# Performance work log

Hardware: AMD Instinct MI355X
Metric: run time of the kernel (lower is better)

## Reference

```python
import jax, jax.numpy as jnp
import numpy as np
from jax import lax

SEQ, BATCH, IN, HID = 4096, 8, 1024, 1024


def setup_inputs() -> dict:
    key = jax.random.key(0)
    k1, k2 = jax.random.split(key)
    X = jax.random.normal(k1, (SEQ, BATCH, IN), dtype=jnp.float32)
    hidden = jnp.zeros((BATCH, HID), dtype=jnp.float32)  # None init == zeros
    W = jax.random.normal(k2, (3 * HID, IN), dtype=jnp.float32) * 0.02
    b = jnp.zeros((3 * HID,), dtype=jnp.float32)
    return {"X": X, "hidden": hidden, "W": W, "b": b}


def reference(X, hidden, W, b):
    # window=1: source = X; Y = Linear(X) -> [S, B, 3H]
    Y = jnp.einsum('sbi,hi->sbh', X, W) + b
    Z, F, O = jnp.split(Y, 3, axis=2)
    Z = jnp.tanh(Z)
    F = jax.nn.sigmoid(F)

    # ForgetMult: c_t = f_t * z_t + (1 - f_t) * c_{t-1}
    def step(c, fz):
        f, z = fz
        c = f * z + (1.0 - f) * c
        return c, c

    _, C = lax.scan(step, hidden, (F, Z))  # C: [S, B, H]
    H = jax.nn.sigmoid(O) * C
    return (H, C[-1:, :, :], C)
```

## Files before the change

### kernel.cpp

```cpp
#include <hip/hip_runtime.h>
#include <hip/hip_bf16.h>
#include <stdint.h>

#define S_   4096
#define B_   8
#define IN_  1024
#define H_   1024
#define M_   (S_ * B_)
#define N_   (3 * H_)
#define K_   IN_
#define CH_  (B_ * H_)
#define NC_  256
#define T_   (S_ / NC_)
#define STRD (CH_ / 4)

typedef unsigned short u16;
typedef __bf16 bf16x8 __attribute__((ext_vector_type(8)));
typedef float  f32x4  __attribute__((ext_vector_type(4)));

__device__ __forceinline__ u16 f2bf(float f) {
  unsigned u = __float_as_uint(f);
  u += 0x7fffu + ((u >> 16) & 1u);
  return (u16)(u >> 16);
}

__device__ __forceinline__ float sigmoid_(float x) { return 1.0f / (1.0f + __expf(-x)); }
__device__ __forceinline__ float tanh_(float x)    { return 2.0f / (1.0f + __expf(-2.0f * x)) - 1.0f; }

__global__ void cvt_all(const float* __restrict__ X, const float* __restrict__ W,
                        u16* __restrict__ Xb, u16* __restrict__ Wb) {
  const int nX = M_ * K_ / 8, nW = N_ * K_ / 8;
  int i = blockIdx.x * blockDim.x + threadIdx.x;
  const float* in; u16* out; int j;
  if (i < nX)           { in = X; out = Xb; j = i; }
  else if (i < nX + nW) { in = W; out = Wb; j = i - nX; }
  else return;
  const float4* p = (const float4*)in;
  float4 a = p[2 * j], b = p[2 * j + 1];
  alignas(16) u16 us[8] = {f2bf(a.x), f2bf(a.y), f2bf(a.z), f2bf(a.w),
                           f2bf(b.x), f2bf(b.y), f2bf(b.z), f2bf(b.w)};
  ((uint4*)out)[j] = *(const uint4*)us;
}

#define SWZ(x) ((x) ^ (((x) >> 3) & 0x30))

#define DS_A(s, h, mh) do {                                                    \
  const char* base_ = (const char*)As_[(s)*2+(h)];                             \
  af[0] = *(const bf16x8*)(base_ + aoff[mh][0]);                               \
  af[1] = *(const bf16x8*)(base_ + aoff[mh][1]);                               \
  af[2] = *(const bf16x8*)(base_ + aoff[mh][2]);                               \
  af[3] = *(const bf16x8*)(base_ + aoff[mh][3]);                               \
} while (0)

#define DS_B(s, h) do {                                                        \
  const char* base_ = (const char*)Bs_[(s)*2+(h)];                             \
  bfr[0] = *(const bf16x8*)(base_ + boff[0]);                                  \
  bfr[1] = *(const bf16x8*)(base_ + boff[1]);                                  \
  bfr[2] = *(const bf16x8*)(base_ + boff[2]);                                  \
  bfr[3] = *(const bf16x8*)(base_ + boff[3]);                                  \
} while (0)

#define MMA(mh) do {                                                           \
  __builtin_amdgcn_s_setprio(1);                                              \
  _Pragma("unroll")                                                            \
  for (int fi_ = 0; fi_ < 4; ++fi_)                                            \
    _Pragma("unroll")                                                          \
    for (int fj_ = 0; fj_ < 4; ++fj_)                                          \
      acc[(mh)*4+fi_][fj_] = __builtin_amdgcn_mfma_f32_16x16x32_bf16(          \
          af[fi_], bfr[fj_], acc[(mh)*4+fi_][fj_], 0, 0, 0);                   \
  __builtin_amdgcn_s_setprio(0);                                              \
} while (0)

#define PH_SYNC() do {                                                         \
  asm volatile("" ::: "memory");                                               \
  __builtin_amdgcn_s_barrier();                                                \
  asm volatile("s_waitcnt lgkmcnt(0)" ::: "memory");                           \
} while (0)

#define PH_END() do {                                                          \
  asm volatile("" ::: "memory");                                               \
  __builtin_amdgcn_s_barrier();                                                \
} while (0)

#define VW(n) asm volatile("s_waitcnt vmcnt(" #n ")" ::: "memory")

__global__ __launch_bounds__(512, 2) void gemm_act(
    const u16* __restrict__ Ab, const u16* __restrict__ Bb,
    const float* __restrict__ bias,
    float* __restrict__ zt,
    float* __restrict__ Cf,
    float* __restrict__ Ho) {
  __shared__ alignas(16) u16 As_[4][8192];
  __shared__ alignas(16) u16 Bs_[4][8192];

  const int tid = threadIdx.x;
  const int w = tid >> 6, l = tid & 63;
  const int m0 = blockIdx.y * 256, n0 = blockIdx.x * 256;
  const int wmo = (w >> 2) * 128, wno = (w & 3) * 64;
  const int lr = l & 15, lq = l >> 4;

  const int D0b  = w * 1024 + l * 16;
  const int row0 = D0b >> 6;
  const int c0   = (SWZ(D0b) & 63) >> 1;

  int aoff[2][4], boff[4];
#pragma unroll
  for (int mh = 0; mh < 2; ++mh)
#pragma unroll
    for (int fi = 0; fi < 4; ++fi)
      aoff[mh][fi] = SWZ((wmo + (mh * 4 + fi) * 16 + lr) * 64 + lq * 16);
#pragma unroll
  for (int fj = 0; fj < 4; ++fj)
    boff[fj] = SWZ((wno + fj * 16 + lr) * 64 + lq * 16);

  auto stage = [&](const u16* __restrict__ G, int rb, int tt, int hh, u16* dstp) {
    const u16* s0 = G + (size_t)(rb + row0) * K_ + (tt * 64 + hh * 32 + c0);
    __builtin_amdgcn_global_load_lds(
        (const __attribute__((address_space(1))) void*)s0,
        (__attribute__((address_space(3))) void*)(dstp + (D0b >> 1)), 16, 0, 0);
    const u16* s1 = s0 + (size_t)128 * K_;
    __builtin_amdgcn_global_load_lds(
        (const __attribute__((address_space(1))) void*)s1,
        (__attribute__((address_space(3))) void*)(dstp + (D0b >> 1) + 4096), 16, 0, 0);
  };

  f32x4 acc[8][4] = {};
  bf16x8 af[4], bfr[4];

  stage(Ab, m0, 0, 0, As_[0]); stage(Bb, n0, 0, 0, Bs_[0]);
  stage(Ab, m0, 0, 1, As_[1]); stage(Bb, n0, 0, 1, Bs_[1]);
  stage(Ab, m0, 1, 0, As_[2]); stage(Bb, n0, 1, 0, Bs_[2]);
  VW(4);
  PH_END();

  for (int i = 0; i < 7; ++i) {
    const int t1 = 2 * i + 1, t2 = 2 * i + 2, t3 = 2 * i + 3;
    DS_A(0, 0, 0); DS_B(0, 0); stage(Ab, m0, t1, 1, As_[3]);
    PH_SYNC(); MMA(0); PH_END();
    DS_A(0, 0, 1);             stage(Bb, n0, t1, 1, Bs_[3]);
    PH_SYNC(); MMA(1); PH_END();
    DS_A(0, 1, 0); DS_B(0, 1); stage(Ab, m0, t2, 0, As_[0]);
    PH_SYNC(); MMA(0); PH_END();
    DS_A(0, 1, 1);             stage(Bb, n0, t2, 0, Bs_[0]); VW(4);
    PH_SYNC(); MMA(1); PH_END();
    DS_A(1, 0, 0); DS_B(1, 0); stage(Ab, m0, t2, 1, As_[1]);
    PH_SYNC(); MMA(0); PH_END();
    DS_A(1, 0, 1);             stage(Bb, n0, t2, 1, Bs_[1]);
    PH_SYNC(); MMA(1); PH_END();
    DS_A(1, 1, 0); DS_B(1, 1); stage(Ab, m0, t3, 0, As_[2]);
    PH_SYNC(); MMA(0); PH_END();
    DS_A(1, 1, 1);             stage(Bb, n0, t3, 0, Bs_[2]); VW(4);
    PH_SYNC(); MMA(1); PH_END();
  }

  DS_A(0, 0, 0); DS_B(0, 0); stage(Ab, m0, 15, 1, As_[3]);
  PH_SYNC(); MMA(0); PH_END();
  DS_A(0, 0, 1);             stage(Bb, n0, 15, 1, Bs_[3]);
  PH_SYNC(); MMA(1); PH_END();
  DS_A(0, 1, 0); DS_B(0, 1);
  PH_SYNC(); MMA(0); PH_END();
  DS_A(0, 1, 1); VW(0);
  PH_SYNC(); MMA(1); PH_END();
  DS_A(1, 0, 0); DS_B(1, 0);
  PH_SYNC(); MMA(0); PH_END();
  DS_A(1, 0, 1);
  PH_SYNC(); MMA(1); PH_END();
  DS_A(1, 1, 0); DS_B(1, 1);
  PH_SYNC(); MMA(0); PH_END();
  DS_A(1, 1, 1);
  PH_SYNC(); MMA(1); PH_END();

  const int seg = n0 >> 10;
  const int nh0 = (n0 & 1023) + wno;
  float* dst = (seg == 0) ? zt : (seg == 1 ? Cf : Ho);
#pragma unroll
  for (int fj = 0; fj < 4; ++fj) {
    const int nn = nh0 + fj * 16 + lr;
    const float bv = bias[seg * 1024 + nn];
#pragma unroll
    for (int fi = 0; fi < 8; ++fi) {
#pragma unroll
      for (int rr = 0; rr < 4; ++rr) {
        const int mm = m0 + wmo + fi * 16 + lq * 4 + rr;
        const float v = acc[fi][fj][rr] + bv;
        dst[(size_t)mm * H_ + nn] = (seg == 0) ? tanh_(v) : sigmoid_(v);
      }
    }
  }
}


#define UPDA4(ff, zz) do { float om_;                                          \
  om_ = 1.f - (ff).x; c.x = (ff).x * (zz).x + om_ * c.x; A.x *= om_;           \
  om_ = 1.f - (ff).y; c.y = (ff).y * (zz).y + om_ * c.y; A.y *= om_;           \
  om_ = 1.f - (ff).z; c.z = (ff).z * (zz).z + om_ * c.z; A.z *= om_;           \
  om_ = 1.f - (ff).w; c.w = (ff).w * (zz).w + om_ * c.w; A.w *= om_;           \
} while (0)

#define UPDB4(ff, zz) do {                                                     \
  c.x = (ff).x * (zz).x + (1.f - (ff).x) * c.x;                                \
  c.y = (ff).y * (zz).y + (1.f - (ff).y) * c.y;                                \
  c.z = (ff).z * (zz).z + (1.f - (ff).z) * c.z;                                \
  c.w = (ff).w * (zz).w + (1.f - (ff).w) * c.w;                                \
} while (0)

__global__ void scanA(const float* __restrict__ Cf, const float* __restrict__ zt,
                      float* __restrict__ ckA, float* __restrict__ ckC) {
  const int ch4 = blockIdx.x * 256 + threadIdx.x;
  const int j   = blockIdx.y;
  const float4* __restrict__ Cf4 = (const float4*)Cf;
  const float4* __restrict__ zt4 = (const float4*)zt;
  size_t base = (size_t)j * T_ * STRD + ch4;
  float4 A = {1.f, 1.f, 1.f, 1.f}, c = {0.f, 0.f, 0.f, 0.f};
  float4 f0 = Cf4[base],        z0 = zt4[base];
  float4 f1 = Cf4[base + STRD], z1 = zt4[base + STRD];
#pragma unroll
  for (int tt = 0; tt < T_ - 2; ++tt) {
    const float4 fn = Cf4[base + 2 * STRD];
    const float4 zn = zt4[base + 2 * STRD];
    UPDA4(f0, z0);
    f0 = f1; z0 = z1; f1 = fn; z1 = zn;
    base += STRD;
  }
  UPDA4(f0, z0);
  UPDA4(f1, z1);
  ((float4*)ckA)[(size_t)j * STRD + ch4] = A;
  ((float4*)ckC)[(size_t)j * STRD + ch4] = c;
}

__global__ void scanComb(const float* __restrict__ ckA, const float* __restrict__ ckC,
                         const float* __restrict__ hidden, float* __restrict__ carry) {
  const int ch4 = blockIdx.x * 64 + threadIdx.x;
  const float4* __restrict__ a4 = (const float4*)ckA;
  const float4* __restrict__ c4 = (const float4*)ckC;
  float4* __restrict__ cr4 = (float4*)carry;
  float4 c = ((const float4*)hidden)[ch4];
  float4 A0 = a4[ch4], C0 = c4[ch4];
#pragma unroll 8
  for (int j = 0; j < NC_ - 1; ++j) {
    const float4 A1 = a4[(size_t)(j + 1) * STRD + ch4];
    const float4 C1 = c4[(size_t)(j + 1) * STRD + ch4];
    cr4[(size_t)j * STRD + ch4] = c;
    c.x = C0.x + A0.x * c.x;
    c.y = C0.y + A0.y * c.y;
    c.z = C0.z + A0.z * c.z;
    c.w = C0.w + A0.w * c.w;
    A0 = A1; C0 = C1;
  }
  cr4[(size_t)(NC_ - 1) * STRD + ch4] = c;
}

__global__ void scanB(float* __restrict__ Cf,
                      const float* __restrict__ zt,
                      float* __restrict__ Ho,
                      float* __restrict__ Clast,
                      const float* __restrict__ carry) {
  const int ch4 = blockIdx.x * 256 + threadIdx.x;
  const int j   = blockIdx.y;
  float4* __restrict__ Cf4 = (float4*)Cf;
  const float4* __restrict__ zt4 = (const float4*)zt;
  float4* __restrict__ Ho4 = (float4*)Ho;
  size_t base = (size_t)j * T_ * STRD + ch4;
  float4 c = ((const float4*)carry)[(size_t)j * STRD + ch4];
  float4 f0 = Cf4[base],        z0 = zt4[base],        o0 = Ho4[base];
  float4 f1 = Cf4[base + STRD], z1 = zt4[base + STRD], o1 = Ho4[base + STRD];
#pragma unroll
  for (int tt = 0; tt < T_ - 2; ++tt) {
    const float4 fn = Cf4[base + 2 * STRD];
    const float4 zn = zt4[base + 2 * STRD];
    const float4 on = Ho4[base + 2 * STRD];
    UPDB4(f0, z0);
    Cf4[base] = c;
    Ho4[base] = float4{o0.x * c.x, o0.y * c.y, o0.z * c.z, o0.w * c.w};
    f0 = f1; z0 = z1; o0 = o1; f1 = fn; z1 = zn; o1 = on;
    base += STRD;
  }
  UPDB4(f0, z0);
  Cf4[base] = c;
  Ho4[base] = float4{o0.x * c.x, o0.y * c.y, o0.z * c.z, o0.w * c.w};
  base += STRD;
  UPDB4(f1, z1);
  Cf4[base] = c;
  Ho4[base] = float4{o1.x * c.x, o1.y * c.y, o1.z * c.z, o1.w * c.w};
  if (j == NC_ - 1) ((float4*)Clast)[ch4] = c;
}

extern "C" void kernel_launch(void* const* d_in, const int* in_sizes, int n_in,
                              void* d_out, int out_size, void* d_ws, size_t ws_size,
                              hipStream_t stream) {
  const float* X    = (const float*)d_in[0];
  const float* hid  = (const float*)d_in[1];
  const float* W    = (const float*)d_in[2];
  const float* bias = (const float*)d_in[3];

  float* out   = (float*)d_out;
  float* Ho    = out;
  float* Clast = out + (size_t)M_ * H_;
  float* Cf    = Clast + CH_;

  char* ws = (char*)d_ws;
  u16*  Xb    = (u16*)ws;
  u16*  Wb    = (u16*)(ws + 67108864);
  float* zt   = (float*)(ws + 73400320);
  float* ckA  = (float*)(ws);
  float* ckC  = (float*)(ws + 8388608);
  float* carry= (float*)(ws + 16777216);

  const int nAll = M_ * K_ / 8 + N_ * K_ / 8;
  cvt_all<<<(nAll + 255) / 256, 256, 0, stream>>>(X, W, Xb, Wb);
  gemm_act<<<dim3(N_ / 256, M_ / 256), 512, 0, stream>>>(Xb, Wb, bias, zt, Cf, Ho);
  scanA<<<dim3(CH_ / 1024, NC_), 256, 0, stream>>>(Cf, zt, ckA, ckC);
  scanComb<<<CH_ / 4 / 64, 64, 0, stream>>>(ckA, ckC, hid, carry);
  scanB<<<dim3(CH_ / 1024, NC_), 256, 0, stream>>>(Cf, zt, Ho, Clast, carry);
}
```

Measured before the change: 835.3 us.

## Store gate activations as fp16 and widen scan chunks with 8-wide lanes

The GEMM epilogue now writes the tanh(Z) and sigmoid(F) intermediates as fp16 into separate workspace buffers instead of fp32, cutting the bytes written by the GEMM and read twice by the scan kernels. The scan kernels process 8 channels per thread with fp16 vector loads, and the chunk count drops from 256 to 64, so each thread does longer serial runs with fewer blocks. This lowers memory traffic in the bandwidth-bound scan phases. It costs precision in the recurrence inputs and reduces parallelism per scan launch, with the inner loop no longer fully unrolled.

```diff
diff --git a/kernel.cpp b/kernel.cpp
--- a/kernel.cpp
+++ b/kernel.cpp
@@ -10,13 +10,15 @@
 #define N_   (3 * H_)
 #define K_   IN_
 #define CH_  (B_ * H_)
-#define NC_  256
+#define NC_  64
 #define T_   (S_ / NC_)
-#define STRD (CH_ / 4)
+#define STR8 (CH_ / 8)
+#define STR4 (CH_ / 4)
 
 typedef unsigned short u16;
 typedef __bf16 bf16x8 __attribute__((ext_vector_type(8)));
 typedef float  f32x4  __attribute__((ext_vector_type(4)));
+typedef _Float16 h8   __attribute__((ext_vector_type(8)));
 
 __device__ __forceinline__ u16 f2bf(float f) {
   unsigned u = __float_as_uint(f);
@@ -87,8 +89,8 @@
 __global__ __launch_bounds__(512, 2) void gemm_act(
     const u16* __restrict__ Ab, const u16* __restrict__ Bb,
     const float* __restrict__ bias,
-    float* __restrict__ zt,
-    float* __restrict__ Cf,
+    _Float16* __restrict__ zh,
+    _Float16* __restrict__ fh,
     float* __restrict__ Ho) {
   __shared__ alignas(16) u16 As_[4][8192];
   __shared__ alignas(16) u16 Bs_[4][8192];
@@ -172,7 +174,6 @@
 
   const int seg = n0 >> 10;
   const int nh0 = (n0 & 1023) + wno;
-  float* dst = (seg == 0) ? zt : (seg == 1 ? Cf : Ho);
 #pragma unroll
   for (int fj = 0; fj < 4; ++fj) {
     const int nn = nh0 + fj * 16 + lr;
@@ -183,49 +184,54 @@
       for (int rr = 0; rr < 4; ++rr) {
         const int mm = m0 + wmo + fi * 16 + lq * 4 + rr;
         const float v = acc[fi][fj][rr] + bv;
-        dst[(size_t)mm * H_ + nn] = (seg == 0) ? tanh_(v) : sigmoid_(v);
+        const size_t idx = (size_t)mm * H_ + nn;
+        if (seg == 0)      zh[idx] = (_Float16)tanh_(v);
+        else if (seg == 1) fh[idx] = (_Float16)sigmoid_(v);
+        else               Ho[idx] = sigmoid_(v);
       }
     }
   }
 }
 
 
-#define UPDA4(ff, zz) do { float om_;                                          \
-  om_ = 1.f - (ff).x; c.x = (ff).x * (zz).x + om_ * c.x; A.x *= om_;           \
-  om_ = 1.f - (ff).y; c.y = (ff).y * (zz).y + om_ * c.y; A.y *= om_;           \
-  om_ = 1.f - (ff).z; c.z = (ff).z * (zz).z + om_ * c.z; A.z *= om_;           \
-  om_ = 1.f - (ff).w; c.w = (ff).w * (zz).w + om_ * c.w; A.w *= om_;           \
-} while (0)
-
-#define UPDB4(ff, zz) do {                                                     \
-  c.x = (ff).x * (zz).x + (1.f - (ff).x) * c.x;                                \
-  c.y = (ff).y * (zz).y + (1.f - (ff).y) * c.y;                                \
-  c.z = (ff).z * (zz).z + (1.f - (ff).z) * c.z;                                \
-  c.w = (ff).w * (zz).w + (1.f - (ff).w) * c.w;                                \
-} while (0)
-
-__global__ void scanA(const float* __restrict__ Cf, const float* __restrict__ zt,
+__global__ void scanA(const _Float16* __restrict__ fhp, const _Float16* __restrict__ zhp,
                       float* __restrict__ ckA, float* __restrict__ ckC) {
-  const int ch4 = blockIdx.x * 256 + threadIdx.x;
+  const int ch8 = blockIdx.x * 256 + threadIdx.x;
   const int j   = blockIdx.y;
-  const float4* __restrict__ Cf4 = (const float4*)Cf;
-  const float4* __restrict__ zt4 = (const float4*)zt;
-  size_t base = (size_t)j * T_ * STRD + ch4;
-  float4 A = {1.f, 1.f, 1.f, 1.f}, c = {0.f, 0.f, 0.f, 0.f};
-  float4 f0 = Cf4[base],        z0 = zt4[base];
-  float4 f1 = Cf4[base + STRD], z1 = zt4[base + STRD];
-#pragma unroll
+  const h8* __restrict__ fh = (const h8*)fhp;
+  const h8* __restrict__ zh = (const h8*)zhp;
+  size_t base = (size_t)j * T_ * STR8 + ch8;
+  float A[8], c[8];
+#pragma unroll
+  for (int k = 0; k < 8; ++k) { A[k] = 1.f; c[k] = 0.f; }
+  h8 f0 = fh[base],        z0 = zh[base];
+  h8 f1 = fh[base + STR8], z1 = zh[base + STR8];
   for (int tt = 0; tt < T_ - 2; ++tt) {
-    const float4 fn = Cf4[base + 2 * STRD];
-    const float4 zn = zt4[base + 2 * STRD];
-    UPDA4(f0, z0);
-    f0 = f1; z0 = z1; f1 = fn; z1 = zn;
-    base += STRD;
-  }
-  UPDA4(f0, z0);
-  UPDA4(f1, z1);
-  ((float4*)ckA)[(size_t)j * STRD + ch4] = A;
-  ((float4*)ckC)[(size_t)j * STRD + ch4] = c;
+    const h8 f2 = fh[base + 2 * STR8];
+    const h8 z2 = zh[base + 2 * STR8];
+#pragma unroll
+    for (int k = 0; k < 8; ++k) {
+      const float f = (float)f0[k], z = (float)z0[k], om = 1.f - f;
+      c[k] = f * z + om * c[k]; A[k] *= om;
+    }
+    f0 = f1; z0 = z1; f1 = f2; z1 = z2; base += STR8;
+  }
+#pragma unroll
+  for (int k = 0; k < 8; ++k) {
+    const float f = (float)f0[k], z = (float)z0[k], om = 1.f - f;
+    c[k] = f * z + om * c[k]; A[k] *= om;
+  }
+#pragma unroll
+  for (int k = 0; k < 8; ++k) {
+    const float f = (float)f1[k], z = (float)z1[k], om = 1.f - f;
+    c[k] = f * z + om * c[k]; A[k] *= om;
+  }
+  float4* a4 = (float4*)ckA; float4* c4 = (float4*)ckC;
+  const size_t o4 = (size_t)j * STR4 + ch8 * 2;
+  a4[o4]     = float4{A[0], A[1], A[2], A[3]};
+  a4[o4 + 1] = float4{A[4], A[5], A[6], A[7]};
+  c4[o4]     = float4{c[0], c[1], c[2], c[3]};
+  c4[o4 + 1] = float4{c[4], c[5], c[6], c[7]};
 }
 
 __global__ void scanComb(const float* __restrict__ ckA, const float* __restrict__ ckC,
@@ -238,51 +244,78 @@
   float4 A0 = a4[ch4], C0 = c4[ch4];
 #pragma unroll 8
   for (int j = 0; j < NC_ - 1; ++j) {
-    const float4 A1 = a4[(size_t)(j + 1) * STRD + ch4];
-    const float4 C1 = c4[(size_t)(j + 1) * STRD + ch4];
-    cr4[(size_t)j * STRD + ch4] = c;
+    const float4 A1 = a4[(size_t)(j + 1) * STR4 + ch4];
+    const float4 C1 = c4[(size_t)(j + 1) * STR4 + ch4];
+    cr4[(size_t)j * STR4 + ch4] = c;
     c.x = C0.x + A0.x * c.x;
     c.y = C0.y + A0.y * c.y;
     c.z = C0.z + A0.z * c.z;
     c.w = C0.w + A0.w * c.w;
     A0 = A1; C0 = C1;
   }
-  cr4[(size_t)(NC_ - 1) * STRD + ch4] = c;
-}
-
-__global__ void scanB(float* __restrict__ Cf,
-                      const float* __restrict__ zt,
+  cr4[(size_t)(NC_ - 1) * STR4 + ch4] = c;
+}
+
+__global__ void scanB(const _Float16* __restrict__ fhp, const _Float16* __restrict__ zhp,
+                      float* __restrict__ Cw,
                       float* __restrict__ Ho,
                       float* __restrict__ Clast,
                       const float* __restrict__ carry) {
-  const int ch4 = blockIdx.x * 256 + threadIdx.x;
+  const int ch8 = blockIdx.x * 256 + threadIdx.x;
   const int j   = blockIdx.y;
-  float4* __restrict__ Cf4 = (float4*)Cf;
-  const float4* __restrict__ zt4 = (const float4*)zt;
-  float4* __restrict__ Ho4 = (float4*)Ho;
-  size_t base = (size_t)j * T_ * STRD + ch4;
-  float4 c = ((const float4*)carry)[(size_t)j * STRD + ch4];
-  float4 f0 = Cf4[base],        z0 = zt4[base],        o0 = Ho4[base];
-  float4 f1 = Cf4[base + STRD], z1 = zt4[base + STRD], o1 = Ho4[base + STRD];
-#pragma unroll
+  const h8* __restrict__ fh = (const h8*)fhp;
+  const h8* __restrict__ zh = (const h8*)zhp;
+  float4* __restrict__ H4 = (float4*)Ho;
+  float4* __restrict__ C4 = (float4*)Cw;
+  size_t b8 = (size_t)j * T_ * STR8 + ch8;
+  size_t b4 = (size_t)j * T_ * STR4 + ch8 * 2;
+  const float4 ca = ((const float4*)carry)[(size_t)j * STR4 + ch8 * 2];
+  const float4 cb = ((const float4*)carry)[(size_t)j * STR4 + ch8 * 2 + 1];
+  float c[8] = {ca.x, ca.y, ca.z, ca.w, cb.x, cb.y, cb.z, cb.w};
+  h8 f0 = fh[b8],        z0 = zh[b8];
+  float4 oa0 = H4[b4], ob0 = H4[b4 + 1];
+  h8 f1 = fh[b8 + STR8], z1 = zh[b8 + STR8];
+  float4 oa1 = H4[b4 + STR4], ob1 = H4[b4 + STR4 + 1];
   for (int tt = 0; tt < T_ - 2; ++tt) {
-    const float4 fn = Cf4[base + 2 * STRD];
-    const float4 zn = zt4[base + 2 * STRD];
-    const float4 on = Ho4[base + 2 * STRD];
-    UPDB4(f0, z0);
-    Cf4[base] = c;
-    Ho4[base] = float4{o0.x * c.x, o0.y * c.y, o0.z * c.z, o0.w * c.w};
-    f0 = f1; z0 = z1; o0 = o1; f1 = fn; z1 = zn; o1 = on;
-    base += STRD;
-  }
-  UPDB4(f0, z0);
-  Cf4[base] = c;
-  Ho4[base] = float4{o0.x * c.x, o0.y * c.y, o0.z * c.z, o0.w * c.w};
-  base += STRD;
-  UPDB4(f1, z1);
-  Cf4[base] = c;
-  Ho4[base] = float4{o1.x * c.x, o1.y * c.y, o1.z * c.z, o1.w * c.w};
-  if (j == NC_ - 1) ((float4*)Clast)[ch4] = c;
+    const h8 f2 = fh[b8 + 2 * STR8];
+    const h8 z2 = zh[b8 + 2 * STR8];
+    const float4 oa2 = H4[b4 + 2 * STR4], ob2 = H4[b4 + 2 * STR4 + 1];
+#pragma unroll
+    for (int k = 0; k < 8; ++k) {
+      const float f = (float)f0[k], z = (float)z0[k];
+      c[k] = f * z + (1.f - f) * c[k];
+    }
+    C4[b4]     = float4{c[0], c[1], c[2], c[3]};
+    C4[b4 + 1] = float4{c[4], c[5], c[6], c[7]};
+    H4[b4]     = float4{oa0.x * c[0], oa0.y * c[1], oa0.z * c[2], oa0.w * c[3]};
+    H4[b4 + 1] = float4{ob0.x * c[4], ob0.y * c[5], ob0.z * c[6], ob0.w * c[7]};
+    f0 = f1; z0 = z1; oa0 = oa1; ob0 = ob1;
+    f1 = f2; z1 = z2; oa1 = oa2; ob1 = ob2;
+    b8 += STR8; b4 += STR4;
+  }
+#pragma unroll
+  for (int k = 0; k < 8; ++k) {
+    const float f = (float)f0[k], z = (float)z0[k];
+    c[k] = f * z + (1.f - f) * c[k];
+  }
+  C4[b4]     = float4{c[0], c[1], c[2], c[3]};
+  C4[b4 + 1] = float4{c[4], c[5], c[6], c[7]};
+  H4[b4]     = float4{oa0.x * c[0], oa0.y * c[1], oa0.z * c[2], oa0.w * c[3]};
+  H4[b4 + 1] = float4{ob0.x * c[4], ob0.y * c[5], ob0.z * c[6], ob0.w * c[7]};
+  b4 += STR4;
+#pragma unroll
+  for (int k = 0; k < 8; ++k) {
+    const float f = (float)f1[k], z = (float)z1[k];
+    c[k] = f * z + (1.f - f) * c[k];
+  }
+  C4[b4]     = float4{c[0], c[1], c[2], c[3]};
+  C4[b4 + 1] = float4{c[4], c[5], c[6], c[7]};
+  H4[b4]     = float4{oa1.x * c[0], oa1.y * c[1], oa1.z * c[2], oa1.w * c[3]};
+  H4[b4 + 1] = float4{ob1.x * c[4], ob1.y * c[5], ob1.z * c[6], ob1.w * c[7]};
+  if (j == NC_ - 1) {
+    ((float4*)Clast)[ch8 * 2]     = float4{c[0], c[1], c[2], c[3]};
+    ((float4*)Clast)[ch8 * 2 + 1] = float4{c[4], c[5], c[6], c[7]};
+  }
 }
 
 extern "C" void kernel_launch(void* const* d_in, const int* in_sizes, int n_in,
@@ -299,17 +332,18 @@
   float* Cf    = Clast + CH_;
 
   char* ws = (char*)d_ws;
-  u16*  Xb    = (u16*)ws;
-  u16*  Wb    = (u16*)(ws + 67108864);
-  float* zt   = (float*)(ws + 73400320);
-  float* ckA  = (float*)(ws);
-  float* ckC  = (float*)(ws + 8388608);
-  float* carry= (float*)(ws + 16777216);
+  u16*      Xb  = (u16*)ws;
+  u16*      Wb  = (u16*)(ws + 67108864);
+  _Float16* zh  = (_Float16*)(ws + 73400320);
+  _Float16* fhg = (_Float16*)(ws + 140509184);
+  float* ckA    = (float*)(ws + 207618048);
+  float* ckC    = (float*)(ws + 209715200);
+  float* carry  = (float*)(ws + 211812352);
 
   const int nAll = M_ * K_ / 8 + N_ * K_ / 8;
   cvt_all<<<(nAll + 255) / 256, 256, 0, stream>>>(X, W, Xb, Wb);
-  gemm_act<<<dim3(N_ / 256, M_ / 256), 512, 0, stream>>>(Xb, Wb, bias, zt, Cf, Ho);
-  scanA<<<dim3(CH_ / 1024, NC_), 256, 0, stream>>>(Cf, zt, ckA, ckC);
+  gemm_act<<<dim3(N_ / 256, M_ / 256), 512, 0, stream>>>(Xb, Wb, bias, zh, fhg, Ho);
+  scanA<<<dim3(CH_ / 8 / 256, NC_), 256, 0, stream>>>(fhg, zh, ckA, ckC);
   scanComb<<<CH_ / 4 / 64, 64, 0, stream>>>(ckA, ckC, hid, carry);
-  scanB<<<dim3(CH_ / 1024, NC_), 256, 0, stream>>>(Cf, zt, Ho, Clast, carry);
-}
+  scanB<<<dim3(CH_ / 8 / 256, NC_), 256, 0, stream>>>(fhg, zh, Cf, Ho, Clast, carry);
+}
```

Measured after the change: 770.4 us. 7.8% less time.
